# Kernel optimization log

Hardware: AMD Instinct MI355X
Metric: run time of the kernel (lower is better)

The kernel has to match this reference:

```python
import jax, jax.numpy as jnp
import numpy as np

N_NODES = 50000
N_EDGES = 640000
IN_DIM = 4
HIDDEN = 128
N_LAYERS = 4


def _linear_params(key, fan_in, fan_out):
    kw, kb = jax.random.split(key)
    s = 1.0 / jnp.sqrt(jnp.float32(fan_in))
    W = jax.random.uniform(kw, (fan_in, fan_out), jnp.float32, -s, s)
    b = jax.random.uniform(kb, (fan_out,), jnp.float32, -s, s)
    return W, b


def setup_inputs() -> dict:
    key = jax.random.key(0)
    ks = jax.random.split(key, 8)
    x = jax.random.normal(ks[0], (N_NODES, IN_DIM), jnp.float32)
    edge_index = jax.random.randint(ks[1], (2, N_EDGES), 0, N_NODES, dtype=jnp.int64)
    edge_attr = jax.random.uniform(ks[2], (N_EDGES, 1), jnp.float32)

    W_enc, b_enc = _linear_params(ks[3], IN_DIM, HIDDEN)

    # Per-layer message MLP: Linear(2H+1, H) -> ReLU -> Linear(H, H)
    W1s, b1s, W2s, b2s = [], [], [], []
    lkeys = jax.random.split(ks[4], N_LAYERS)
    for lk in lkeys:
        k1, k2 = jax.random.split(lk)
        W1, b1 = _linear_params(k1, 2 * HIDDEN + 1, HIDDEN)
        W2, b2 = _linear_params(k2, HIDDEN, HIDDEN)
        W1s.append(W1); b1s.append(b1); W2s.append(W2); b2s.append(b2)
    W1 = jnp.stack(W1s); b1 = jnp.stack(b1s)
    W2 = jnp.stack(W2s); b2 = jnp.stack(b2s)

    W_ghost, b_ghost = _linear_params(ks[5], HIDDEN, 1)
    W_period, b_period = _linear_params(ks[6], HIDDEN, 1)
    W_grad, b_grad = _linear_params(ks[7], HIDDEN, 2)

    return {
        "x": x, "edge_index": edge_index, "edge_attr": edge_attr,
        "W_enc": W_enc, "b_enc": b_enc,
        "W1": W1, "b1": b1, "W2": W2, "b2": b2,
        "W_ghost": W_ghost, "b_ghost": b_ghost,
        "W_period": W_period, "b_period": b_period,
        "W_grad": W_grad, "b_grad": b_grad,
    }


def reference(x, edge_index, edge_attr, W_enc, b_enc, W1, b1, W2, b2,
              W_ghost, b_ghost, W_period, b_period, W_grad, b_grad):
    # PyG: x_j = source = edge_index[0], x_i = target = edge_index[1]; aggr='add' at target.
    src = edge_index[0]
    dst = edge_index[1]

    h = x @ W_enc + b_enc  # [N, H]
    for l in range(N_LAYERS):
        # gather -> concat [x_i, x_j, edge_attr] -> 2-layer MLP -> scatter-add
        flow = jnp.concatenate([h[dst], h[src], edge_attr], axis=-1)  # [E, 2H+1]
        msg = jnp.maximum(flow @ W1[l] + b1[l], 0.0) @ W2[l] + b2[l]  # [E, H]
        agg = jax.ops.segment_sum(msg, dst, num_segments=N_NODES)    # [N, H]
        h = jnp.maximum(agg, 0.0)

    ghost_score = jax.nn.sigmoid(h @ W_ghost + b_ghost)  # [N, 1]
    period_pred = h @ W_period + b_period                # [N, 1]
    grad_pred = h @ W_grad + b_grad                      # [N, 2]
    # Note: ghost_locations/ghost_periods in the original are a data-dependent
    # boolean-mask select (not jit-compatible); the mask is derivable from
    # ghost_score/grad_pred, so we return the dense tensors that define it.
    return (h, ghost_score, period_pred, grad_pred)
```

## Files before the change

### kernel.cpp

```cpp
#include <hip/hip_runtime.h>
#include <hip/hip_fp16.h>

#define N_NODES 50000
#define N_EDGES 640000
#define HIDDEN  128
#define N_LAYERS 4
#define TILE_E  128
#define EBLK    (N_EDGES / TILE_E)
#define NCHUNK  196
#define NBLK64  ((N_NODES + 63) / 64)

#define OUT_GHOST  (N_NODES * HIDDEN)
#define OUT_PERIOD (OUT_GHOST + N_NODES)
#define OUT_GRAD   (OUT_PERIOD + N_NODES)

typedef _Float16 f16x8 __attribute__((ext_vector_type(8)));
typedef _Float16 f16x2 __attribute__((ext_vector_type(2)));
typedef float    f32x4 __attribute__((ext_vector_type(4)));

__device__ __forceinline__ int swz(int row, int colbyte) {
    return (row * 256 + colbyte) ^ ((row & 7) << 4);
}

__device__ __forceinline__ int ei_is64(const int* __restrict__ ei) {
    return (ei[1] == 0 && ei[3] == 0 && ei[5] == 0) ? 1 : 0;
}
__device__ __forceinline__ int ei_src(const int* __restrict__ ei, int is64, int e) {
    return is64 ? ei[2 * e] : ei[e];
}
__device__ __forceinline__ int ei_dst(const int* __restrict__ ei, int is64, int e) {
    return is64 ? ei[2 * (N_EDGES + e)] : ei[N_EDGES + e];
}

__global__ void count_kernel(const int* __restrict__ ei, int* __restrict__ counts) {
    int e = blockIdx.x * 256 + threadIdx.x;
    atomicAdd(&counts[ei_dst(ei, ei_is64(ei), e)], 1);
}

__global__ void csr_local_kernel(const int* __restrict__ counts, int* __restrict__ cursor,
                                 int* __restrict__ chunkSum, int* __restrict__ bslot,
                                 _Float16* __restrict__ aggH) {
    __shared__ int buf[256];
    int t = threadIdx.x, i = blockIdx.x * 256 + t;
    int v = (i < N_NODES) ? counts[i] : 0;
    buf[t] = v;
    __syncthreads();
    for (int off = 1; off < 256; off <<= 1) {
        int add = (t >= off) ? buf[t - off] : 0;
        __syncthreads();
        buf[t] += add;
        __syncthreads();
    }
    if (i < N_NODES) {
        cursor[i] = buf[t] - v;
        bslot[i] = -1;
        if (v == 0) {
            float4 z = {0.f, 0.f, 0.f, 0.f};
#pragma unroll
            for (int k = 0; k < 16; ++k)
                *(float4*)&aggH[(size_t)i * 128 + k * 8] = z;
        }
    }
    if (t == 255) chunkSum[blockIdx.x] = buf[255];
}

__global__ void chunk_scan_kernel(const int* __restrict__ chunkSum, int* __restrict__ chunkBase) {
    __shared__ int buf[256];
    int t = threadIdx.x;
    int v = (t < NCHUNK) ? chunkSum[t] : 0;
    buf[t] = v;
    __syncthreads();
    for (int off = 1; off < 256; off <<= 1) {
        int add = (t >= off) ? buf[t - off] : 0;
        __syncthreads();
        buf[t] += add;
        __syncthreads();
    }
    if (t < NCHUNK) chunkBase[t] = buf[t] - v;
}

__global__ void scatter_kernel(const int* __restrict__ ei, const float* __restrict__ ea,
                               const int* __restrict__ chunkBase, int* __restrict__ cursor,
                               uint2* __restrict__ sdPE) {
    int e = blockIdx.x * 256 + threadIdx.x;
    int is64 = ei_is64(ei);
    int s = ei_src(ei, is64, e);
    int d = ei_dst(ei, is64, e);
    int p = chunkBase[d >> 8] + atomicAdd(&cursor[d], 1);
    uint2 v;
    v.x = (unsigned)s | ((unsigned)d << 16);
    v.y = __float_as_uint(ea[e]);
    sdPE[p] = v;
}

__global__ void pack_w_kernel(const float* __restrict__ W1, const float* __restrict__ W2,
                              _Float16* __restrict__ W1c, _Float16* __restrict__ W2p) {
    int id = blockIdx.x * 256 + threadIdx.x;
    if (id < 131072) {
        int j = id & 7, l = (id >> 3) & 63, c = (id >> 9) & 15, kb = (id >> 13) & 3, lay = id >> 15;
        int k = kb * 32 + (l >> 4) * 8 + j, col = c * 16 + (l & 15);
        const float* Wl = W1 + (size_t)lay * 257 * 128;
        W1c[id] = (_Float16)((col < 128) ? Wl[(size_t)k * 128 + col]
                                         : Wl[(size_t)(128 + k) * 128 + (col - 128)]);
    } else if (id < 196608) {
        int id2 = id - 131072;
        int j = id2 & 7, l = (id2 >> 3) & 63, c = (id2 >> 9) & 7, kb = (id2 >> 12) & 3, lay = id2 >> 14;
        int k = kb * 32 + (l >> 4) * 8 + j, col = c * 16 + (l & 15);
        W2p[id2] = (_Float16)W2[(size_t)lay * 128 * 128 + (size_t)k * 128 + col];
    }
}

__global__ void bnd_setup_kernel(const uint2* __restrict__ sdPE, int* __restrict__ bslot) {
    int t = blockIdx.x * 256 + threadIdx.x;
    if (t >= 1 && t < EBLK) {
        unsigned dp = sdPE[t * TILE_E - 1].x >> 16;
        unsigned d0 = sdPE[t * TILE_E].x >> 16;
        if (dp == d0) bslot[d0] = t;
    }
}

__global__ __launch_bounds__(512, 8)
void edge_gather_kernel(const _Float16* __restrict__ PQ,
                        const uint2* __restrict__ sdPE,
                        const float* __restrict__ w1last,
                        _Float16* __restrict__ aggH, float* __restrict__ agg32c) {
    __shared__ __align__(16) unsigned char tile[TILE_E * 256];
    __shared__ int dstL[TILE_E];
    __shared__ int srcL[TILE_E];
    __shared__ _Float16 eaL[TILE_E];
    __shared__ int segStart[TILE_E + 1];
    __shared__ int nsegS, contP, contN;

    const int tid = threadIdx.x;
    const int bid = (blockIdx.x & 7) * (EBLK / 8) + (blockIdx.x >> 3);
    const int e_base = bid * TILE_E;

    if (tid < TILE_E) {
        uint2 u = sdPE[e_base + tid];
        srcL[tid] = (int)(u.x & 0xFFFFu);
        dstL[tid] = (int)(u.x >> 16);
        eaL[tid]  = (_Float16)__uint_as_float(u.y);
    } else if (tid == TILE_E) {
        contP = (e_base > 0 && (sdPE[e_base - 1].x >> 16) == (sdPE[e_base].x >> 16)) ? 1 : 0;
    } else if (tid == TILE_E + 1) {
        contN = (e_base + TILE_E < N_EDGES &&
                 (sdPE[e_base + TILE_E - 1].x >> 16) == (sdPE[e_base + TILE_E].x >> 16)) ? 1 : 0;
    }
    __syncthreads();

    if (tid < 128) {
        int lane = tid & 63;
        int fl_lo = (lane == 0) ? 1 : (dstL[lane] != dstL[lane - 1]);
        unsigned long long m0 = __ballot(fl_lo);
        if (tid < 64) {
            if (fl_lo) segStart[__popcll(m0 & ((1ull << lane) - 1))] = lane;
        } else {
            int j = 64 + lane;
            int fl = (dstL[j] != dstL[j - 1]);
            unsigned long long m1 = __ballot(fl);
            int nlo = __popcll(m0);
            if (fl) segStart[nlo + __popcll(m1 & ((1ull << lane) - 1))] = j;
            if (lane == 0) {
                int ns = nlo + __popcll(m1);
                nsegS = ns;
                segStart[ns] = TILE_E;
            }
        }
    }

    {
        const int t16 = tid & 15, rg = tid >> 4;
        const int c8 = t16 * 8;

        f16x8 pv[4], qv[4];
#pragma unroll
        for (int rr = 0; rr < 4; ++rr) {
            int row = rg + 32 * rr;
            pv[rr] = *(const f16x8*)&PQ[(size_t)dstL[row] * 256 + c8];
            qv[rr] = *(const f16x8*)&PQ[(size_t)srcL[row] * 256 + 128 + c8];
        }

        f16x8 wl8, z8;
#pragma unroll
        for (int j = 0; j < 8; ++j) {
            wl8[j] = (_Float16)w1last[c8 + j];
            z8[j]  = (_Float16)0.f;
        }

#pragma unroll
        for (int rr = 0; rr < 4; ++rr) {
            int row = rg + 32 * rr;
            f16x8 t = pv[rr] + qv[rr] + wl8 * eaL[row];
            f16x8 hv = __builtin_elementwise_max(t, z8);
            *(f16x8*)(tile + swz(row, c8 * 2)) = hv;
        }
    }
    __syncthreads();

    {
        int col2 = (tid & 63) * 2, sh = tid >> 6;
        int ns = nsegS, cP = contP, cN = contN;
        for (int s = sh; s < ns; s += 8) {
            int b = segStart[s], en = segStart[s + 1];
            float s0 = 0.f, s1 = 0.f;
            for (int e2 = b; e2 < en; ++e2) {
                f16x2 hv = *(const f16x2*)(tile + swz(e2, col2 * 2));
                s0 += (float)hv[0];
                s1 += (float)hv[1];
            }
            bool isP = (s == 0 && cP), isN = (s == ns - 1 && cN);
            if (isP || isN) {
                int slot = isP ? bid : bid + 1;
                atomicAdd(&agg32c[(size_t)slot * 128 + col2], s0);
                atomicAdd(&agg32c[(size_t)slot * 128 + col2 + 1], s1);
            } else {
                int node = dstL[b];
                f16x2 o; o[0] = (_Float16)s0; o[1] = (_Float16)s1;
                *(f16x2*)&aggH[(size_t)node * 128 + col2] = o;
            }
        }
    }
}

__global__ __launch_bounds__(512, 6)
void node_layer_kernel(const _Float16* __restrict__ aggH,
                       const int* __restrict__ counts,
                       const int* __restrict__ bslot, float* __restrict__ agg32c,
                       const _Float16* __restrict__ W2p, const float* __restrict__ b2,
                       const _Float16* __restrict__ W1c, const float* __restrict__ b1n,
                       _Float16* __restrict__ PQ, float* __restrict__ out,
                       const float* __restrict__ Wg, const float* __restrict__ bg,
                       const float* __restrict__ Wp, const float* __restrict__ bp,
                       const float* __restrict__ Wr, const float* __restrict__ br,
                       int last) {
    __shared__ __align__(16) unsigned char tile[64 * 256];
    __shared__ int degL[64];
    __shared__ float hw[512];

    const int tid = threadIdx.x;
    const int base = blockIdx.x * 64;

    {
        const int t16 = tid & 15, rg = tid >> 4;
#pragma unroll
        for (int rr = 0; rr < 2; ++rr) {
            int row = rg + 32 * rr;
            int n = base + row;
            f16x8 v = {0, 0, 0, 0, 0, 0, 0, 0};
            if (n < N_NODES) {
                int bs = bslot[n];
                if (bs >= 0) {
                    float* ap = &agg32c[(size_t)bs * 128 + t16 * 8];
                    float4 a = *(const float4*)ap;
                    float4 b = *(const float4*)(ap + 4);
                    v[0] = (_Float16)a.x; v[1] = (_Float16)a.y;
                    v[2] = (_Float16)a.z; v[3] = (_Float16)a.w;
                    v[4] = (_Float16)b.x; v[5] = (_Float16)b.y;
                    v[6] = (_Float16)b.z; v[7] = (_Float16)b.w;
                    float4 z = {0.f, 0.f, 0.f, 0.f};
                    *(float4*)ap = z; *(float4*)(ap + 4) = z;
                } else {
                    v = *(const f16x8*)&aggH[(size_t)n * 128 + t16 * 8];
                }
            }
            *(f16x8*)(tile + swz(row, t16 * 16)) = v;
        }
        if (tid < 64) degL[tid] = (base + tid < N_NODES) ? counts[base + tid] : 0;
        if (last) {
            if (tid < 128)       hw[tid] = Wg[tid];
            else if (tid < 256)  hw[tid] = Wp[tid - 128];
            else                 hw[tid] = Wr[tid - 256];
        }
    }
    __syncthreads();

    const int w = tid >> 6, l = tid & 63, l16 = l & 15, lg = l >> 4;

    f32x4 acc[4];
#pragma unroll
    for (int rt = 0; rt < 4; ++rt) acc[rt] = (f32x4){0.f, 0.f, 0.f, 0.f};
    const f16x8* W2v = (const f16x8*)W2p;
#pragma unroll
    for (int kb = 0; kb < 4; ++kb) {
        f16x8 bf = W2v[(kb * 8 + w) * 64 + l];
#pragma unroll
        for (int rt = 0; rt < 4; ++rt) {
            f16x8 a = *(const f16x8*)(tile + swz(rt * 16 + l16, kb * 64 + lg * 16));
            acc[rt] = __builtin_amdgcn_mfma_f32_16x16x32_f16(a, bf, acc[rt], 0, 0, 0);
        }
    }
    __syncthreads();

    {
        int col = 16 * w + l16;
        float bias = b2[col];
#pragma unroll
        for (int rt = 0; rt < 4; ++rt)
#pragma unroll
            for (int r = 0; r < 4; ++r) {
                int row = rt * 16 + lg * 4 + r;
                float h = fmaxf(acc[rt][r] + (float)degL[row] * bias, 0.f);
                *(_Float16*)(tile + swz(row, col * 2)) = (_Float16)h;
                if (last && base + row < N_NODES)
                    out[(size_t)(base + row) * 128 + col] = h;
            }
    }
    __syncthreads();

    if (last) {
        int r = tid >> 3, part = tid & 7;
        float sg = 0.f, sp = 0.f, s0 = 0.f, s1 = 0.f;
#pragma unroll
        for (int i = 0; i < 8; ++i) {
            int c = part * 16 + i * 2;
            f16x2 hv = *(const f16x2*)(tile + swz(r, c * 2));
            float h0 = (float)hv[0], h1 = (float)hv[1];
            sg += h0 * hw[c] + h1 * hw[c + 1];
            sp += h0 * hw[128 + c] + h1 * hw[128 + c + 1];
            s0 += h0 * hw[256 + c * 2] + h1 * hw[256 + (c + 1) * 2];
            s1 += h0 * hw[256 + c * 2 + 1] + h1 * hw[256 + (c + 1) * 2 + 1];
        }
        sg += __shfl_xor(sg, 1); sg += __shfl_xor(sg, 2); sg += __shfl_xor(sg, 4);
        sp += __shfl_xor(sp, 1); sp += __shfl_xor(sp, 2); sp += __shfl_xor(sp, 4);
        s0 += __shfl_xor(s0, 1); s0 += __shfl_xor(s0, 2); s0 += __shfl_xor(s0, 4);
        s1 += __shfl_xor(s1, 1); s1 += __shfl_xor(s1, 2); s1 += __shfl_xor(s1, 4);
        int n = base + r;
        if (part == 0 && n < N_NODES) {
            float g = sg + bg[0];
            out[OUT_GHOST + n]        = 1.f / (1.f + expf(-g));
            out[OUT_PERIOD + n]       = sp + bp[0];
            out[OUT_GRAD + n * 2]     = s0 + br[0];
            out[OUT_GRAD + n * 2 + 1] = s1 + br[1];
        }
        return;
    }

    f32x4 acc2[2][4];
#pragma unroll
    for (int ci = 0; ci < 2; ++ci)
#pragma unroll
        for (int rt = 0; rt < 4; ++rt) acc2[ci][rt] = (f32x4){0.f, 0.f, 0.f, 0.f};
    const f16x8* W1v = (const f16x8*)W1c;
#pragma unroll
    for (int kb = 0; kb < 4; ++kb) {
        f16x8 b0  = W1v[(kb * 16 + 2 * w) * 64 + l];
        f16x8 b1f = W1v[(kb * 16 + 2 * w + 1) * 64 + l];
#pragma unroll
        for (int rt = 0; rt < 4; ++rt) {
            f16x8 a = *(const f16x8*)(tile + swz(rt * 16 + l16, kb * 64 + lg * 16));
            acc2[0][rt] = __builtin_amdgcn_mfma_f32_16x16x32_f16(a, b0,  acc2[0][rt], 0, 0, 0);
            acc2[1][rt] = __builtin_amdgcn_mfma_f32_16x16x32_f16(a, b1f, acc2[1][rt], 0, 0, 0);
        }
    }
#pragma unroll
    for (int ci = 0; ci < 2; ++ci) {
        int col = (2 * w + ci) * 16 + l16;
        float bb = (col < 128) ? b1n[col] : 0.f;
#pragma unroll
        for (int rt = 0; rt < 4; ++rt)
#pragma unroll
            for (int r = 0; r < 4; ++r) {
                int row = rt * 16 + lg * 4 + r;
                if (base + row < N_NODES)
                    PQ[(size_t)(base + row) * 256 + col] = (_Float16)(acc2[ci][rt][r] + bb);
            }
    }
}

__global__ __launch_bounds__(512, 6)
void node_enc_kernel(const float* __restrict__ x,
                     const float* __restrict__ Wenc, const float* __restrict__ benc,
                     const _Float16* __restrict__ W1c, const float* __restrict__ b1n,
                     _Float16* __restrict__ PQ) {
    __shared__ __align__(16) unsigned char tile[64 * 256];
    const int tid = threadIdx.x;
    const int base = blockIdx.x * 64;

    {
        const int t16 = tid & 15, rg = tid >> 4;
        const int c8 = t16 * 8;
        float wv[4][8], bv[8];
#pragma unroll
        for (int i = 0; i < 4; ++i) {
            float4 a = *(const float4*)&Wenc[i * 128 + c8];
            float4 b = *(const float4*)&Wenc[i * 128 + c8 + 4];
            wv[i][0] = a.x; wv[i][1] = a.y; wv[i][2] = a.z; wv[i][3] = a.w;
            wv[i][4] = b.x; wv[i][5] = b.y; wv[i][6] = b.z; wv[i][7] = b.w;
        }
        float4 ba = *(const float4*)&benc[c8];
        float4 bb = *(const float4*)&benc[c8 + 4];
        bv[0] = ba.x; bv[1] = ba.y; bv[2] = ba.z; bv[3] = ba.w;
        bv[4] = bb.x; bv[5] = bb.y; bv[6] = bb.z; bv[7] = bb.w;
#pragma unroll
        for (int rr = 0; rr < 2; ++rr) {
            int row = rg + 32 * rr;
            float4 xr = {0.f, 0.f, 0.f, 0.f};
            if (base + row < N_NODES) xr = *(const float4*)&x[(size_t)(base + row) * 4];
            f16x8 hv;
#pragma unroll
            for (int j = 0; j < 8; ++j) {
                float v = bv[j] + xr.x * wv[0][j] + xr.y * wv[1][j] + xr.z * wv[2][j] + xr.w * wv[3][j];
                hv[j] = (_Float16)v;
            }
            *(f16x8*)(tile + swz(row, c8 * 2)) = hv;
        }
    }
    __syncthreads();

    const int w = tid >> 6, l = tid & 63, l16 = l & 15, lg = l >> 4;
    f32x4 acc2[2][4];
#pragma unroll
    for (int ci = 0; ci < 2; ++ci)
#pragma unroll
        for (int rt = 0; rt < 4; ++rt) acc2[ci][rt] = (f32x4){0.f, 0.f, 0.f, 0.f};
    const f16x8* W1v = (const f16x8*)W1c;
#pragma unroll
    for (int kb = 0; kb < 4; ++kb) {
        f16x8 b0  = W1v[(kb * 16 + 2 * w) * 64 + l];
        f16x8 b1f = W1v[(kb * 16 + 2 * w + 1) * 64 + l];
#pragma unroll
        for (int rt = 0; rt < 4; ++rt) {
            f16x8 a = *(const f16x8*)(tile + swz(rt * 16 + l16, kb * 64 + lg * 16));
            acc2[0][rt] = __builtin_amdgcn_mfma_f32_16x16x32_f16(a, b0,  acc2[0][rt], 0, 0, 0);
            acc2[1][rt] = __builtin_amdgcn_mfma_f32_16x16x32_f16(a, b1f, acc2[1][rt], 0, 0, 0);
        }
    }
#pragma unroll
    for (int ci = 0; ci < 2; ++ci) {
        int col = (2 * w + ci) * 16 + l16;
        float bb = (col < 128) ? b1n[col] : 0.f;
#pragma unroll
        for (int rt = 0; rt < 4; ++rt)
#pragma unroll
            for (int r = 0; r < 4; ++r) {
                int row = rt * 16 + lg * 4 + r;
                if (base + row < N_NODES)
                    PQ[(size_t)(base + row) * 256 + col] = (_Float16)(acc2[ci][rt][r] + bb);
            }
    }
}

extern "C" void kernel_launch(void* const* d_in, const int* in_sizes, int n_in,
                              void* d_out, int out_size, void* d_ws, size_t ws_size,
                              hipStream_t stream) {
    const float* x     = (const float*)d_in[0];
    const int*   ei    = (const int*)d_in[1];
    const float* ea    = (const float*)d_in[2];
    const float* W_enc = (const float*)d_in[3];
    const float* b_enc = (const float*)d_in[4];
    const float* W1    = (const float*)d_in[5];
    const float* b1    = (const float*)d_in[6];
    const float* W2    = (const float*)d_in[7];
    const float* b2    = (const float*)d_in[8];
    const float* Wg    = (const float*)d_in[9];
    const float* bg    = (const float*)d_in[10];
    const float* Wp    = (const float*)d_in[11];
    const float* bp    = (const float*)d_in[12];
    const float* Wr    = (const float*)d_in[13];
    const float* br    = (const float*)d_in[14];

    float* out = (float*)d_out;

    char* ws = (char*)d_ws;
    _Float16*     PQ     = (_Float16*)ws;     ws += (size_t)N_NODES * 256 * 2;
    _Float16*     aggH   = (_Float16*)ws;     ws += (size_t)N_NODES * 128 * 2;
    float*        agg32c = (float*)ws;        ws += (size_t)EBLK * 128 * 4;
    uint2*        sdPE   = (uint2*)ws;        ws += (size_t)N_EDGES * 8;
    int*          counts = (int*)ws;          ws += 200192;
    int*          cursor = (int*)ws;          ws += 200192;
    int*          bslot  = (int*)ws;          ws += 200192;
    _Float16*     W1c    = (_Float16*)ws;     ws += (size_t)131072 * 2;
    _Float16*     W2p    = (_Float16*)ws;     ws += (size_t)65536 * 2;
    int*          chunkSum  = (int*)ws;       ws += 1024;
    int*          chunkBase = (int*)ws;       ws += 1024;

    hipMemsetAsync(counts, 0, (size_t)N_NODES * 4, stream);
    hipMemsetAsync(agg32c, 0, (size_t)EBLK * 128 * 4, stream);

    count_kernel<<<N_EDGES / 256, 256, 0, stream>>>(ei, counts);
    csr_local_kernel<<<NCHUNK, 256, 0, stream>>>(counts, cursor, chunkSum, bslot, aggH);
    chunk_scan_kernel<<<1, 256, 0, stream>>>(chunkSum, chunkBase);
    scatter_kernel<<<N_EDGES / 256, 256, 0, stream>>>(ei, ea, chunkBase, cursor, sdPE);

    pack_w_kernel<<<196608 / 256, 256, 0, stream>>>(W1, W2, W1c, W2p);
    bnd_setup_kernel<<<(EBLK + 255) / 256, 256, 0, stream>>>(sdPE, bslot);

    node_enc_kernel<<<NBLK64, 512, 0, stream>>>(x, W_enc, b_enc, W1c, b1, PQ);

    for (int l = 0; l < N_LAYERS; ++l) {
        edge_gather_kernel<<<EBLK, 512, 0, stream>>>(
            PQ, sdPE,
            W1 + (size_t)l * 257 * 128 + 256 * 128,
            aggH, agg32c);
        int nl = (l < 3) ? (l + 1) : 0;
        node_layer_kernel<<<NBLK64, 512, 0, stream>>>(
            aggH, counts, bslot, agg32c,
            W2p + (size_t)l * 16384, b2 + l * HIDDEN,
            W1c + (size_t)nl * 32768, b1 + nl * HIDDEN,
            PQ, out, Wg, bg, Wp, bp, Wr, br,
            (l == N_LAYERS - 1) ? 1 : 0);
    }
}
```

Measured before the change: 312.9 us.

## Split CSR build atomics into 8 classes and two-pass sliced edge scatter

Degree counting and cursor atomics are split into 8 per-class arrays selected by block index, with per-class cursor offsets derived in the local scan. Edge scatter becomes two kernels: one computes each edge's destination slot and packed payload, and a second writes them out in 8 position slices so each pass targets a narrower address range. This aims to reduce atomic contention and scattered-write locality costs in CSR construction, at the price of a larger memset, extra buffers, an extra launch, and eightfold re-reading of the slot array.

```diff
diff --git a/kernel.cpp b/kernel.cpp
--- a/kernel.cpp
+++ b/kernel.cpp
@@ -9,6 +9,8 @@
 #define EBLK    (N_EDGES / TILE_E)
 #define NCHUNK  196
 #define NBLK64  ((N_NODES + 63) / 64)
+#define NC      50048
+#define PSLICE  (N_EDGES / 8)
 
 #define OUT_GHOST  (N_NODES * HIDDEN)
 #define OUT_PERIOD (OUT_GHOST + N_NODES)
@@ -32,17 +34,26 @@
     return is64 ? ei[2 * (N_EDGES + e)] : ei[N_EDGES + e];
 }
 
-__global__ void count_kernel(const int* __restrict__ ei, int* __restrict__ counts) {
+__global__ void count_kernel(const int* __restrict__ ei, int* __restrict__ counts8) {
     int e = blockIdx.x * 256 + threadIdx.x;
-    atomicAdd(&counts[ei_dst(ei, ei_is64(ei), e)], 1);
-}
-
-__global__ void csr_local_kernel(const int* __restrict__ counts, int* __restrict__ cursor,
-                                 int* __restrict__ chunkSum, int* __restrict__ bslot,
+    int cls = blockIdx.x & 7;
+    atomicAdd(&counts8[cls * NC + ei_dst(ei, ei_is64(ei), e)], 1);
+}
+
+__global__ void csr_local_kernel(const int* __restrict__ counts8,
+                                 int* __restrict__ deg,
+                                 int* __restrict__ cursorClass,
+                                 int* __restrict__ chunkSum,
+                                 int* __restrict__ bslot,
                                  _Float16* __restrict__ aggH) {
     __shared__ int buf[256];
     int t = threadIdx.x, i = blockIdx.x * 256 + t;
-    int v = (i < N_NODES) ? counts[i] : 0;
+    int c8[8]; int v = 0;
+#pragma unroll
+    for (int c = 0; c < 8; ++c) {
+        c8[c] = (i < N_NODES) ? counts8[c * NC + i] : 0;
+        v += c8[c];
+    }
     buf[t] = v;
     __syncthreads();
     for (int off = 1; off < 256; off <<= 1) {
@@ -52,7 +63,10 @@
         __syncthreads();
     }
     if (i < N_NODES) {
-        cursor[i] = buf[t] - v;
+        int run = buf[t] - v;
+#pragma unroll
+        for (int c = 0; c < 8; ++c) { cursorClass[c * NC + i] = run; run += c8[c]; }
+        deg[i] = v;
         bslot[i] = -1;
         if (v == 0) {
             float4 z = {0.f, 0.f, 0.f, 0.f};
@@ -79,18 +93,28 @@
     if (t < NCHUNK) chunkBase[t] = buf[t] - v;
 }
 
-__global__ void scatter_kernel(const int* __restrict__ ei, const float* __restrict__ ea,
-                               const int* __restrict__ chunkBase, int* __restrict__ cursor,
-                               uint2* __restrict__ sdPE) {
+__global__ void rankA_kernel(const int* __restrict__ ei, const float* __restrict__ ea,
+                             const int* __restrict__ chunkBase, int* __restrict__ cursorClass,
+                             int* __restrict__ pArr, uint2* __restrict__ packedArr) {
     int e = blockIdx.x * 256 + threadIdx.x;
+    int cls = blockIdx.x & 7;
     int is64 = ei_is64(ei);
     int s = ei_src(ei, is64, e);
     int d = ei_dst(ei, is64, e);
-    int p = chunkBase[d >> 8] + atomicAdd(&cursor[d], 1);
+    int p = chunkBase[d >> 8] + atomicAdd(&cursorClass[cls * NC + d], 1);
+    pArr[e] = p;
     uint2 v;
     v.x = (unsigned)s | ((unsigned)d << 16);
     v.y = __float_as_uint(ea[e]);
-    sdPE[p] = v;
+    packedArr[e] = v;
+}
+
+__global__ void rankB_kernel(const int* __restrict__ pArr, const uint2* __restrict__ packedArr,
+                             uint2* __restrict__ sdPE) {
+    int r = blockIdx.x & 7;
+    int e = (blockIdx.x >> 3) * 256 + threadIdx.x;
+    int p = pArr[e];
+    if ((unsigned)p / PSLICE == (unsigned)r) sdPE[p] = packedArr[e];
 }
 
 __global__ void pack_w_kernel(const float* __restrict__ W1, const float* __restrict__ W2,
@@ -224,7 +248,7 @@
 
 __global__ __launch_bounds__(512, 6)
 void node_layer_kernel(const _Float16* __restrict__ aggH,
-                       const int* __restrict__ counts,
+                       const int* __restrict__ deg,
                        const int* __restrict__ bslot, float* __restrict__ agg32c,
                        const _Float16* __restrict__ W2p, const float* __restrict__ b2,
                        const _Float16* __restrict__ W1c, const float* __restrict__ b1n,
@@ -265,7 +289,7 @@
             }
             *(f16x8*)(tile + swz(row, t16 * 16)) = v;
         }
-        if (tid < 64) degL[tid] = (base + tid < N_NODES) ? counts[base + tid] : 0;
+        if (tid < 64) degL[tid] = (base + tid < N_NODES) ? deg[base + tid] : 0;
         if (last) {
             if (tid < 128)       hw[tid] = Wg[tid];
             else if (tid < 256)  hw[tid] = Wp[tid - 128];
@@ -462,25 +486,29 @@
     float* out = (float*)d_out;
 
     char* ws = (char*)d_ws;
-    _Float16*     PQ     = (_Float16*)ws;     ws += (size_t)N_NODES * 256 * 2;
-    _Float16*     aggH   = (_Float16*)ws;     ws += (size_t)N_NODES * 128 * 2;
-    float*        agg32c = (float*)ws;        ws += (size_t)EBLK * 128 * 4;
-    uint2*        sdPE   = (uint2*)ws;        ws += (size_t)N_EDGES * 8;
-    int*          counts = (int*)ws;          ws += 200192;
-    int*          cursor = (int*)ws;          ws += 200192;
-    int*          bslot  = (int*)ws;          ws += 200192;
-    _Float16*     W1c    = (_Float16*)ws;     ws += (size_t)131072 * 2;
-    _Float16*     W2p    = (_Float16*)ws;     ws += (size_t)65536 * 2;
+    _Float16*     PQ        = (_Float16*)ws;  ws += (size_t)N_NODES * 256 * 2;
+    _Float16*     aggH      = (_Float16*)ws;  ws += (size_t)N_NODES * 128 * 2;
+    float*        agg32c    = (float*)ws;     ws += (size_t)EBLK * 128 * 4;
+    uint2*        sdPE      = (uint2*)ws;     ws += (size_t)N_EDGES * 8;
+    uint2*        packedArr = (uint2*)ws;     ws += (size_t)N_EDGES * 8;
+    int*          pArr      = (int*)ws;       ws += (size_t)N_EDGES * 4;
+    int*          counts8   = (int*)ws;       ws += (size_t)8 * NC * 4;
+    int*          cursorC   = (int*)ws;       ws += (size_t)8 * NC * 4;
+    int*          deg       = (int*)ws;       ws += (size_t)NC * 4;
+    int*          bslot     = (int*)ws;       ws += (size_t)NC * 4;
+    _Float16*     W1c       = (_Float16*)ws;  ws += (size_t)131072 * 2;
+    _Float16*     W2p       = (_Float16*)ws;  ws += (size_t)65536 * 2;
     int*          chunkSum  = (int*)ws;       ws += 1024;
     int*          chunkBase = (int*)ws;       ws += 1024;
 
-    hipMemsetAsync(counts, 0, (size_t)N_NODES * 4, stream);
+    hipMemsetAsync(counts8, 0, (size_t)8 * NC * 4, stream);
     hipMemsetAsync(agg32c, 0, (size_t)EBLK * 128 * 4, stream);
 
-    count_kernel<<<N_EDGES / 256, 256, 0, stream>>>(ei, counts);
-    csr_local_kernel<<<NCHUNK, 256, 0, stream>>>(counts, cursor, chunkSum, bslot, aggH);
+    count_kernel<<<N_EDGES / 256, 256, 0, stream>>>(ei, counts8);
+    csr_local_kernel<<<NCHUNK, 256, 0, stream>>>(counts8, deg, cursorC, chunkSum, bslot, aggH);
     chunk_scan_kernel<<<1, 256, 0, stream>>>(chunkSum, chunkBase);
-    scatter_kernel<<<N_EDGES / 256, 256, 0, stream>>>(ei, ea, chunkBase, cursor, sdPE);
+    rankA_kernel<<<N_EDGES / 256, 256, 0, stream>>>(ei, ea, chunkBase, cursorC, pArr, packedArr);
+    rankB_kernel<<<8 * (N_EDGES / 256), 256, 0, stream>>>(pArr, packedArr, sdPE);
 
     pack_w_kernel<<<196608 / 256, 256, 0, stream>>>(W1, W2, W1c, W2p);
     bnd_setup_kernel<<<(EBLK + 255) / 256, 256, 0, stream>>>(sdPE, bslot);
@@ -494,7 +522,7 @@
             aggH, agg32c);
         int nl = (l < 3) ? (l + 1) : 0;
         node_layer_kernel<<<NBLK64, 512, 0, stream>>>(
-            aggH, counts, bslot, agg32c,
+            aggH, deg, bslot, agg32c,
             W2p + (size_t)l * 16384, b2 + l * HIDDEN,
             W1c + (size_t)nl * 32768, b1 + nl * HIDDEN,
             PQ, out, Wg, bg, Wp, bp, Wr, br,
```

Measured after the change: 309.9 us. No clear change (-1.0%).
